# Performance work log

Measured on AMD Instinct MI355X. Metric: run time of the kernel, lower is better.

The kernel has to match this reference:

```python
import jax, jax.numpy as jnp
import numpy as np

K = 512  # number of clusters
D = 128  # feature dim
N = 8192 # number of points


def setup_inputs() -> dict:
    key = jax.random.key(0)
    k1, k2 = jax.random.split(key)
    locF = jax.random.normal(k1, (N, 1, D), dtype=jnp.float32)
    Ck = jax.random.normal(k2, (1, K, D), dtype=jnp.float32)
    return {"locF": locF, "Ck": Ck}


def reference(locF, Ck):
    # locF: [N, 1, D], Ck: [1, K, D]
    x = locF[:, 0, :]          # [N, D]
    c = Ck[0]                  # [K, D]
    # (GEMM expansion avoids the [N, K, D] broadcast; argmin is unchanged)
    d2 = ((x * x).sum(-1, keepdims=True)
          - 2.0 * (x @ c.T)
          + (c * c).sum(-1)[None, :]) / D   # [N, K]
    index = jnp.argmin(d2, axis=1)           # [N]
    # per-cluster scatter-sum and counts (fused, single pass)
    Ck1 = jax.ops.segment_sum(x, index, num_segments=K)[None]  # [1, K, D]
    nItems = jax.ops.segment_sum(jnp.ones((x.shape[0],), dtype=jnp.int32),
                                 index, num_segments=K).reshape(1, -1)  # [1, K]
    return (Ck1, nItems)
```

## Files before the change

### kernel.cpp

```cpp
#include <hip/hip_runtime.h>
#include <hip/hip_bf16.h>

#define KC 512
#define DD 128
#define NP 8192


__global__ __launch_bounds__(256) void kprep(const float* __restrict__ Ck,
                                             float* __restrict__ CkT,
                                             float* __restrict__ sumc2,
                                             float* __restrict__ out) {
    const int b = blockIdx.x;
    const int t = threadIdx.x;
    if (b < 64) {
        const float4 v = *(const float4*)(Ck + b * 1024 + t * 4);
        const int k = b * 8 + (t >> 5);
        const int d = (t & 31) * 4;
        CkT[(d + 0) * KC + k] = v.x;
        CkT[(d + 1) * KC + k] = v.y;
        CkT[(d + 2) * KC + k] = v.z;
        CkT[(d + 3) * KC + k] = v.w;
    } else if (b == 64) {
        #pragma unroll
        for (int c = 0; c < 2; ++c) {
            const int k = t + c * 256;
            const float4* row = (const float4*)(Ck + k * DD);
            float s = 0.f;
            #pragma unroll
            for (int i = 0; i < 32; ++i) {
                const float4 v = row[i];
                s += v.x * v.x + v.y * v.y + v.z * v.z + v.w * v.w;
            }
            sumc2[k] = s;
        }
    } else {
        const int base = (b - 65) * 2048 + t;
        #pragma unroll
        for (int i = 0; i < 8; ++i) {
            const int idx = base + i * 256;
            if (idx < KC * DD + KC) out[idx] = 0.f;
        }
    }
}

__global__ __launch_bounds__(128) void kmain(const float* __restrict__ X,
                                             const float* __restrict__ CkT,
                                             const float* __restrict__ sumc2,
                                             float* __restrict__ out) {
    __shared__ __align__(16) float xs[8 * DD];
    __shared__ float bvx[2][8];
    __shared__ int   bix[2][8];
    __shared__ int   win[8];

    const int tid  = threadIdx.x;
    const int lane = tid & 63;
    const int h    = tid >> 6;
    const int p0   = blockIdx.x * 8;

    {
        const float4* Xv = (const float4*)(X + p0 * DD);
        float4* xv = (float4*)xs;
        xv[tid]       = Xv[tid];
        xv[tid + 128] = Xv[tid + 128];
    }
    __syncthreads();

    const float* cp = CkT + h * 256 + 4 * lane;

    float4 cn[4], cc[4];
    #pragma unroll
    for (int dd = 0; dd < 4; ++dd) cn[dd] = *(const float4*)(cp + dd * KC);

    float acc[8][4];
    #pragma unroll
    for (int p = 0; p < 8; ++p)
        #pragma unroll
        for (int j = 0; j < 4; ++j) acc[p][j] = 0.f;

    #pragma unroll 4
    for (int t = 0; t < 32; ++t) {
        #pragma unroll
        for (int dd = 0; dd < 4; ++dd) cc[dd] = cn[dd];
        if (t < 31) {
            #pragma unroll
            for (int dd = 0; dd < 4; ++dd)
                cn[dd] = *(const float4*)(cp + ((t + 1) * 4 + dd) * KC);
        }
        float4 xf[8];
        #pragma unroll
        for (int p = 0; p < 8; ++p)
            xf[p] = *(const float4*)&xs[p * DD + t * 4];
        #pragma unroll
        for (int dd = 0; dd < 4; ++dd) {
            #pragma unroll
            for (int p = 0; p < 8; ++p) {
                const float xv = (&xf[p].x)[dd];
                acc[p][0] = fmaf(xv, cc[dd].x, acc[p][0]);
                acc[p][1] = fmaf(xv, cc[dd].y, acc[p][1]);
                acc[p][2] = fmaf(xv, cc[dd].z, acc[p][2]);
                acc[p][3] = fmaf(xv, cc[dd].w, acc[p][3]);
            }
        }
    }

    float bestv[8];
    int   besti[8];
    #pragma unroll
    for (int p = 0; p < 8; ++p) { bestv[p] = 3.4e38f; besti[p] = 0; }
    const float4 s2v = *(const float4*)(sumc2 + h * 256 + 4 * lane);
    #pragma unroll
    for (int j = 0; j < 4; ++j) {
        const int cent = h * 256 + 4 * lane + j;
        const float s2 = (&s2v.x)[j];
        #pragma unroll
        for (int p = 0; p < 8; ++p) {
            const float v = fmaf(-2.f, acc[p][j], s2);
            if (v < bestv[p]) { bestv[p] = v; besti[p] = cent; }
        }
    }
    #pragma unroll
    for (int off = 1; off < 64; off <<= 1) {
        #pragma unroll
        for (int p = 0; p < 8; ++p) {
            const float ov = __shfl_xor(bestv[p], off);
            const int   oi = __shfl_xor(besti[p], off);
            if (ov < bestv[p] || (ov == bestv[p] && oi < besti[p])) {
                bestv[p] = ov; besti[p] = oi;
            }
        }
    }
    if (lane == 0) {
        #pragma unroll
        for (int p = 0; p < 8; ++p) { bvx[h][p] = bestv[p]; bix[h][p] = besti[p]; }
    }
    __syncthreads();
    if (tid < 8) {
        const float v0 = bvx[0][tid], v1 = bvx[1][tid];
        win[tid] = (v1 < v0) ? bix[1][tid] : bix[0][tid];
    }
    __syncthreads();

    #pragma unroll
    for (int i = 0; i < 8; ++i) {
        const int flat = tid + 128 * i;
        const int p = flat >> 7;
        const int d = flat & 127;
        atomicAdd(&out[win[p] * DD + d], xs[flat]);
    }
    if (tid < 8) atomicAdd(&out[KC * DD + win[tid]], 1.0f);
}

extern "C" void kernel_launch(void* const* d_in, const int* in_sizes, int n_in,
                              void* d_out, int out_size, void* d_ws, size_t ws_size,
                              hipStream_t stream) {
    const float* locF = (const float*)d_in[0];
    const float* Ck   = (const float*)d_in[1];
    float* out   = (float*)d_out;
    float* sumc2 = (float*)d_ws;
    float* CkT   = (float*)((char*)d_ws + 4096);

    hipLaunchKernelGGL(kprep, dim3(98), dim3(256), 0, stream, Ck, CkT, sumc2, out);
    hipLaunchKernelGGL(kmain, dim3(1024), dim3(128), 0, stream, locF, CkT, sumc2, out);
}
```

Baseline: 41.59 us.

## Retile distance GEMM to 16 points per block with 2 centroids per lane

Each block now handles 16 points with 256 threads, and each lane covers 2 centroids instead of 4, so each centroid value loaded from global memory is reused across twice as many points. The centroid prefetch becomes a two-stage buffer that loads two d-steps ahead. The goal is to halve the CkT global traffic per point and hide load latency better. In exchange the block count is halved, there is a four-way cross-wave reduction, and each thread does more LDS reads per FMA.

```diff
diff --git a/kernel.cpp b/kernel.cpp
--- a/kernel.cpp
+++ b/kernel.cpp
@@ -43,85 +43,89 @@
     }
 }
 
-__global__ __launch_bounds__(128) void kmain(const float* __restrict__ X,
+__global__ __launch_bounds__(256) void kmain(const float* __restrict__ X,
                                              const float* __restrict__ CkT,
                                              const float* __restrict__ sumc2,
                                              float* __restrict__ out) {
-    __shared__ __align__(16) float xs[8 * DD];
-    __shared__ float bvx[2][8];
-    __shared__ int   bix[2][8];
-    __shared__ int   win[8];
+    __shared__ __align__(16) float xs[16 * DD];
+    __shared__ float bvw[4][16];
+    __shared__ int   biw[4][16];
+    __shared__ int   win[16];
 
     const int tid  = threadIdx.x;
     const int lane = tid & 63;
-    const int h    = tid >> 6;
-    const int p0   = blockIdx.x * 8;
+    const int w    = tid >> 6;
+    const int p0   = blockIdx.x * 16;
+    const int c0   = w * 128 + 2 * lane;
 
     {
         const float4* Xv = (const float4*)(X + p0 * DD);
         float4* xv = (float4*)xs;
         xv[tid]       = Xv[tid];
-        xv[tid + 128] = Xv[tid + 128];
+        xv[tid + 256] = Xv[tid + 256];
     }
     __syncthreads();
 
-    const float* cp = CkT + h * 256 + 4 * lane;
+    const float* cp = CkT + c0;
 
-    float4 cn[4], cc[4];
+    float2 cb[2][4];
     #pragma unroll
-    for (int dd = 0; dd < 4; ++dd) cn[dd] = *(const float4*)(cp + dd * KC);
+    for (int dd = 0; dd < 4; ++dd) cb[0][dd] = *(const float2*)(cp + (0 + dd) * KC);
+    #pragma unroll
+    for (int dd = 0; dd < 4; ++dd) cb[1][dd] = *(const float2*)(cp + (4 + dd) * KC);
 
-    float acc[8][4];
+    float acc[16][2];
     #pragma unroll
-    for (int p = 0; p < 8; ++p)
+    for (int p = 0; p < 16; ++p) { acc[p][0] = 0.f; acc[p][1] = 0.f; }
+
+    #pragma unroll 2
+    for (int t = 0; t < 32; ++t) {
+        const int b = t & 1;
+        float2 cc[4];
         #pragma unroll
-        for (int j = 0; j < 4; ++j) acc[p][j] = 0.f;
-
-    #pragma unroll 4
-    for (int t = 0; t < 32; ++t) {
-        #pragma unroll
-        for (int dd = 0; dd < 4; ++dd) cc[dd] = cn[dd];
-        if (t < 31) {
+        for (int dd = 0; dd < 4; ++dd) cc[dd] = cb[b][dd];
+        if (t < 30) {
             #pragma unroll
             for (int dd = 0; dd < 4; ++dd)
-                cn[dd] = *(const float4*)(cp + ((t + 1) * 4 + dd) * KC);
+                cb[b][dd] = *(const float2*)(cp + ((t + 2) * 4 + dd) * KC);
         }
-        float4 xf[8];
         #pragma unroll
-        for (int p = 0; p < 8; ++p)
-            xf[p] = *(const float4*)&xs[p * DD + t * 4];
-        #pragma unroll
-        for (int dd = 0; dd < 4; ++dd) {
+        for (int half = 0; half < 2; ++half) {
+            float4 xf[8];
             #pragma unroll
-            for (int p = 0; p < 8; ++p) {
-                const float xv = (&xf[p].x)[dd];
-                acc[p][0] = fmaf(xv, cc[dd].x, acc[p][0]);
-                acc[p][1] = fmaf(xv, cc[dd].y, acc[p][1]);
-                acc[p][2] = fmaf(xv, cc[dd].z, acc[p][2]);
-                acc[p][3] = fmaf(xv, cc[dd].w, acc[p][3]);
+            for (int i = 0; i < 8; ++i)
+                xf[i] = *(const float4*)&xs[(half * 8 + i) * DD + t * 4];
+            #pragma unroll
+            for (int dd = 0; dd < 4; ++dd) {
+                #pragma unroll
+                for (int i = 0; i < 8; ++i) {
+                    const int p = half * 8 + i;
+                    const float xv = (&xf[i].x)[dd];
+                    acc[p][0] = fmaf(xv, cc[dd].x, acc[p][0]);
+                    acc[p][1] = fmaf(xv, cc[dd].y, acc[p][1]);
+                }
             }
         }
     }
 
-    float bestv[8];
-    int   besti[8];
+    float bestv[16];
+    int   besti[16];
     #pragma unroll
-    for (int p = 0; p < 8; ++p) { bestv[p] = 3.4e38f; besti[p] = 0; }
-    const float4 s2v = *(const float4*)(sumc2 + h * 256 + 4 * lane);
+    for (int p = 0; p < 16; ++p) { bestv[p] = 3.4e38f; besti[p] = 0; }
+    const float2 s2 = *(const float2*)(sumc2 + c0);
     #pragma unroll
-    for (int j = 0; j < 4; ++j) {
-        const int cent = h * 256 + 4 * lane + j;
-        const float s2 = (&s2v.x)[j];
+    for (int j = 0; j < 2; ++j) {
+        const float s2j = (&s2.x)[j];
         #pragma unroll
-        for (int p = 0; p < 8; ++p) {
-            const float v = fmaf(-2.f, acc[p][j], s2);
-            if (v < bestv[p]) { bestv[p] = v; besti[p] = cent; }
+        for (int p = 0; p < 16; ++p) {
+            const float v = fmaf(-2.f, acc[p][j], s2j);
+            if (v < bestv[p]) { bestv[p] = v; besti[p] = c0 + j; }
         }
     }
     #pragma unroll
     for (int off = 1; off < 64; off <<= 1) {
         #pragma unroll
-        for (int p = 0; p < 8; ++p) {
+        for (int p = 0; p < 16; ++p) {
             const float ov = __shfl_xor(bestv[p], off);
             const int   oi = __shfl_xor(besti[p], off);
             if (ov < bestv[p] || (ov == bestv[p] && oi < besti[p])) {
@@ -131,23 +135,30 @@
     }
     if (lane == 0) {
         #pragma unroll
-        for (int p = 0; p < 8; ++p) { bvx[h][p] = bestv[p]; bix[h][p] = besti[p]; }
+        for (int p = 0; p < 16; ++p) { bvw[w][p] = bestv[p]; biw[w][p] = besti[p]; }
     }
     __syncthreads();
-    if (tid < 8) {
-        const float v0 = bvx[0][tid], v1 = bvx[1][tid];
-        win[tid] = (v1 < v0) ? bix[1][tid] : bix[0][tid];
+    if (tid < 16) {
+        float bv = bvw[0][tid];
+        int   bi = biw[0][tid];
+        #pragma unroll
+        for (int w2 = 1; w2 < 4; ++w2) {
+            const float v = bvw[w2][tid];
+            const int   i2 = biw[w2][tid];
+            if (v < bv) { bv = v; bi = i2; }
+        }
+        win[tid] = bi;
     }
     __syncthreads();
 
     #pragma unroll
     for (int i = 0; i < 8; ++i) {
-        const int flat = tid + 128 * i;
+        const int flat = tid + 256 * i;
         const int p = flat >> 7;
         const int d = flat & 127;
         atomicAdd(&out[win[p] * DD + d], xs[flat]);
     }
-    if (tid < 8) atomicAdd(&out[KC * DD + win[tid]], 1.0f);
+    if (tid < 16) atomicAdd(&out[KC * DD + win[tid]], 1.0f);
 }
 
 extern "C" void kernel_launch(void* const* d_in, const int* in_sizes, int n_in,
@@ -160,5 +171,5 @@
     float* CkT   = (float*)((char*)d_ws + 4096);
 
     hipLaunchKernelGGL(kprep, dim3(98), dim3(256), 0, stream, Ck, CkT, sumc2, out);
-    hipLaunchKernelGGL(kmain, dim3(1024), dim3(128), 0, stream, locF, CkT, sumc2, out);
+    hipLaunchKernelGGL(kmain, dim3(512), dim3(256), 0, stream, locF, CkT, sumc2, out);
 }
```

Measured after the change: 50.09 us. 20.4% more time.

## Replace atomic scatter-add with counting-sort and per-cluster gather reduction

Applied to the files above, without the earlier changes.

Removes the per-point global float atomicAdd scatter of feature vectors into cluster sums. The assignment kernel now only writes indices. A single-block kernel builds a histogram and exclusive scan, then buckets point ids by cluster. A gather kernel then sums each cluster's points without atomics. This avoids atomic contention and drops the output zeroing, but adds two launches and a serial single-block ordering stage.

```diff
diff --git a/kernel.cpp b/kernel.cpp
--- a/kernel.cpp
+++ b/kernel.cpp
@@ -8,8 +8,7 @@
 
 __global__ __launch_bounds__(256) void kprep(const float* __restrict__ Ck,
                                              float* __restrict__ CkT,
-                                             float* __restrict__ sumc2,
-                                             float* __restrict__ out) {
+                                             float* __restrict__ sumc2) {
     const int b = blockIdx.x;
     const int t = threadIdx.x;
     if (b < 64) {
@@ -20,7 +19,7 @@
         CkT[(d + 1) * KC + k] = v.y;
         CkT[(d + 2) * KC + k] = v.z;
         CkT[(d + 3) * KC + k] = v.w;
-    } else if (b == 64) {
+    } else {
         #pragma unroll
         for (int c = 0; c < 2; ++c) {
             const int k = t + c * 256;
@@ -33,24 +32,16 @@
             }
             sumc2[k] = s;
         }
-    } else {
-        const int base = (b - 65) * 2048 + t;
-        #pragma unroll
-        for (int i = 0; i < 8; ++i) {
-            const int idx = base + i * 256;
-            if (idx < KC * DD + KC) out[idx] = 0.f;
-        }
-    }
-}
-
-__global__ __launch_bounds__(128) void kmain(const float* __restrict__ X,
-                                             const float* __restrict__ CkT,
-                                             const float* __restrict__ sumc2,
-                                             float* __restrict__ out) {
+    }
+}
+
+__global__ __launch_bounds__(128) void kassign(const float* __restrict__ X,
+                                               const float* __restrict__ CkT,
+                                               const float* __restrict__ sumc2,
+                                               int* __restrict__ idxout) {
     __shared__ __align__(16) float xs[8 * DD];
     __shared__ float bvx[2][8];
     __shared__ int   bix[2][8];
-    __shared__ int   win[8];
 
     const int tid  = threadIdx.x;
     const int lane = tid & 63;
@@ -136,18 +127,80 @@
     __syncthreads();
     if (tid < 8) {
         const float v0 = bvx[0][tid], v1 = bvx[1][tid];
-        win[tid] = (v1 < v0) ? bix[1][tid] : bix[0][tid];
-    }
-    __syncthreads();
-
-    #pragma unroll
-    for (int i = 0; i < 8; ++i) {
-        const int flat = tid + 128 * i;
-        const int p = flat >> 7;
-        const int d = flat & 127;
-        atomicAdd(&out[win[p] * DD + d], xs[flat]);
-    }
-    if (tid < 8) atomicAdd(&out[KC * DD + win[tid]], 1.0f);
+        idxout[p0 + tid] = (v1 < v0) ? bix[1][tid] : bix[0][tid];
+    }
+}
+
+__global__ __launch_bounds__(512) void korder(const int* __restrict__ idx,
+                                              int* __restrict__ order,
+                                              int* __restrict__ cnts,
+                                              int* __restrict__ offs,
+                                              float* __restrict__ out) {
+    __shared__ int hist[KC];
+    __shared__ int scan[KC];
+    __shared__ int cur[KC];
+    const int t = threadIdx.x;
+
+    hist[t] = 0;
+    __syncthreads();
+
+    int myidx[16];
+    #pragma unroll
+    for (int i = 0; i < 16; ++i) {
+        myidx[i] = idx[t + 512 * i];
+        atomicAdd(&hist[myidx[i]], 1);
+    }
+    __syncthreads();
+
+    const int c = hist[t];
+    out[KC * DD + t] = (float)c;
+    cnts[t] = c;
+
+    scan[t] = c;
+    __syncthreads();
+    for (int off = 1; off < KC; off <<= 1) {
+        const int add = (t >= off) ? scan[t - off] : 0;
+        __syncthreads();
+        scan[t] += add;
+        __syncthreads();
+    }
+    const int excl = scan[t] - c;
+    offs[t] = excl;
+    cur[t]  = excl;
+    __syncthreads();
+
+    #pragma unroll
+    for (int i = 0; i < 16; ++i) {
+        const int p = t + 512 * i;
+        const int slot = atomicAdd(&cur[myidx[i]], 1);
+        order[slot] = p;
+    }
+}
+
+__global__ __launch_bounds__(128) void kgather(const float* __restrict__ X,
+                                               const int* __restrict__ order,
+                                               const int* __restrict__ cnts,
+                                               const int* __restrict__ offs,
+                                               float* __restrict__ out) {
+    const int k = blockIdx.x;
+    const int d = threadIdx.x;
+    const int cnt = cnts[k];
+    const int off = offs[k];
+
+    float s0 = 0.f, s1 = 0.f, s2 = 0.f, s3 = 0.f;
+    int i = 0;
+    for (; i + 4 <= cnt; i += 4) {
+        const int pa = order[off + i + 0];
+        const int pb = order[off + i + 1];
+        const int pc = order[off + i + 2];
+        const int pd = order[off + i + 3];
+        s0 += X[pa * DD + d];
+        s1 += X[pb * DD + d];
+        s2 += X[pc * DD + d];
+        s3 += X[pd * DD + d];
+    }
+    for (; i < cnt; ++i) s0 += X[order[off + i] * DD + d];
+    out[k * DD + d] = (s0 + s1) + (s2 + s3);
 }
 
 extern "C" void kernel_launch(void* const* d_in, const int* in_sizes, int n_in,
@@ -156,9 +209,16 @@
     const float* locF = (const float*)d_in[0];
     const float* Ck   = (const float*)d_in[1];
     float* out   = (float*)d_out;
-    float* sumc2 = (float*)d_ws;
-    float* CkT   = (float*)((char*)d_ws + 4096);
-
-    hipLaunchKernelGGL(kprep, dim3(98), dim3(256), 0, stream, Ck, CkT, sumc2, out);
-    hipLaunchKernelGGL(kmain, dim3(1024), dim3(128), 0, stream, locF, CkT, sumc2, out);
-}
+    char*  ws    = (char*)d_ws;
+    float* sumc2 = (float*)(ws);
+    float* CkT   = (float*)(ws + 4096);
+    int*   idx   = (int*)(ws + 266240);
+    int*   order = (int*)(ws + 299008);
+    int*   cnts  = (int*)(ws + 331776);
+    int*   offs  = (int*)(ws + 333824);
+
+    hipLaunchKernelGGL(kprep,   dim3(65),   dim3(256), 0, stream, Ck, CkT, sumc2);
+    hipLaunchKernelGGL(kassign, dim3(1024), dim3(128), 0, stream, locF, CkT, sumc2, idx);
+    hipLaunchKernelGGL(korder,  dim3(1),    dim3(512), 0, stream, idx, order, cnts, offs, out);
+    hipLaunchKernelGGL(kgather, dim3(512),  dim3(128), 0, stream, locF, order, cnts, offs, out);
+}
```

Result: slower. 67.13 us (+61.4%).

## Replace per-point atomic scatter with counting-sort by cluster and segmented gather-sum

Applied to the files above, without the earlier changes.

The old version had every point atomically add its 128 features into its cluster row. This replaces that with a counting sort. The assign kernel records each point's cluster and a rank in per-(cluster, block-group) counters. A single-block scan then builds offsets, the counts output and a sorted (point, cluster) list. A gather kernel sums runs of equal clusters and issues one atomic per run per feature. The aim is to cut float-atomic contention and volume, at the cost of two extra kernel launches and a serial single-block scan.

```diff
diff --git a/kernel.cpp b/kernel.cpp
--- a/kernel.cpp
+++ b/kernel.cpp
@@ -9,7 +9,8 @@
 __global__ __launch_bounds__(256) void kprep(const float* __restrict__ Ck,
                                              float* __restrict__ CkT,
                                              float* __restrict__ sumc2,
-                                             float* __restrict__ out) {
+                                             float* __restrict__ out,
+                                             int* __restrict__ cnts2) {
     const int b = blockIdx.x;
     const int t = threadIdx.x;
     if (b < 64) {
@@ -33,24 +34,26 @@
             }
             sumc2[k] = s;
         }
+    } else if (b < 97) {
+        float* dst = out + (b - 65) * 2048;
+        #pragma unroll
+        for (int i = 0; i < 8; ++i) dst[t + 256 * i] = 0.f;
     } else {
-        const int base = (b - 65) * 2048 + t;
-        #pragma unroll
-        for (int i = 0; i < 8; ++i) {
-            const int idx = base + i * 256;
-            if (idx < KC * DD + KC) out[idx] = 0.f;
-        }
-    }
-}
-
-__global__ __launch_bounds__(128) void kmain(const float* __restrict__ X,
-                                             const float* __restrict__ CkT,
-                                             const float* __restrict__ sumc2,
-                                             float* __restrict__ out) {
+        int* dst = cnts2 + (b - 97) * 2048;
+        #pragma unroll
+        for (int i = 0; i < 8; ++i) dst[t + 256 * i] = 0;
+    }
+}
+
+__global__ __launch_bounds__(128) void kassign(const float* __restrict__ X,
+                                               const float* __restrict__ CkT,
+                                               const float* __restrict__ sumc2,
+                                               int* __restrict__ idxout,
+                                               int* __restrict__ rank2,
+                                               int* __restrict__ cnts2) {
     __shared__ __align__(16) float xs[8 * DD];
     __shared__ float bvx[2][8];
     __shared__ int   bix[2][8];
-    __shared__ int   win[8];
 
     const int tid  = threadIdx.x;
     const int lane = tid & 63;
@@ -136,18 +139,100 @@
     __syncthreads();
     if (tid < 8) {
         const float v0 = bvx[0][tid], v1 = bvx[1][tid];
-        win[tid] = (v1 < v0) ? bix[1][tid] : bix[0][tid];
-    }
-    __syncthreads();
-
+        const int c = (v1 < v0) ? bix[1][tid] : bix[0][tid];
+        const int p = p0 + tid;
+        idxout[p] = c;
+        rank2[p] = atomicAdd(&cnts2[c * 64 + (blockIdx.x & 63)], 1);
+    }
+}
+
+__global__ __launch_bounds__(1024) void kscan(const int* __restrict__ cnts2,
+                                              const int* __restrict__ idx,
+                                              const int* __restrict__ rank2,
+                                              int* __restrict__ offsflat,
+                                              int2* __restrict__ sorted,
+                                              float* __restrict__ out) {
+    __shared__ int sex[1024];
+    const int t = threadIdx.x;
+
+    int arr[32];
+    {
+        const int4* src = (const int4*)cnts2 + t * 8;
+        #pragma unroll
+        for (int i = 0; i < 8; ++i) {
+            const int4 v = src[i];
+            arr[4 * i + 0] = v.x; arr[4 * i + 1] = v.y;
+            arr[4 * i + 2] = v.z; arr[4 * i + 3] = v.w;
+        }
+    }
+    int loc[32];
+    int tot = 0;
+    #pragma unroll
+    for (int i = 0; i < 32; ++i) { loc[i] = tot; tot += arr[i]; }
+
+    sex[t] = tot;
+    __syncthreads();
+    for (int off = 1; off < 1024; off <<= 1) {
+        const int a = (t >= off) ? sex[t - off] : 0;
+        __syncthreads();
+        sex[t] += a;
+        __syncthreads();
+    }
+    const int excl = sex[t] - tot;
+
+    {
+        int4* dst = (int4*)offsflat + t * 8;
+        #pragma unroll
+        for (int i = 0; i < 8; ++i)
+            dst[i] = make_int4(excl + loc[4 * i + 0], excl + loc[4 * i + 1],
+                               excl + loc[4 * i + 2], excl + loc[4 * i + 3]);
+    }
+
+    __syncthreads();
+    sex[t] = excl;
+    __syncthreads();
+    if (t < 512) {
+        const int start = sex[2 * t];
+        const int end   = (t == 511) ? NP : sex[2 * t + 2];
+        out[KC * DD + t] = (float)(end - start);
+    }
+
+    __syncthreads();
     #pragma unroll
     for (int i = 0; i < 8; ++i) {
-        const int flat = tid + 128 * i;
-        const int p = flat >> 7;
-        const int d = flat & 127;
-        atomicAdd(&out[win[p] * DD + d], xs[flat]);
-    }
-    if (tid < 8) atomicAdd(&out[KC * DD + win[tid]], 1.0f);
+        const int p = t + 1024 * i;
+        const int c = idx[p];
+        const int g = (p >> 3) & 63;
+        const int s0 = offsflat[c * 64 + g] + rank2[p];
+        sorted[s0] = make_int2(p, c);
+    }
+}
+
+__global__ __launch_bounds__(128) void kgather(const float* __restrict__ X,
+                                               const int2* __restrict__ sorted,
+                                               float* __restrict__ out) {
+    const int d  = threadIdx.x;
+    const int s0 = blockIdx.x * 16;
+
+    int2 pc[16];
+    #pragma unroll
+    for (int i = 0; i < 16; ++i) pc[i] = sorted[s0 + i];
+
+    float xr[16];
+    #pragma unroll
+    for (int i = 0; i < 16; ++i) xr[i] = X[pc[i].x * DD + d];
+
+    float sum = 0.f;
+    #pragma unroll
+    for (int i = 0; i < 15; ++i) {
+        sum += xr[i];
+        if (pc[i + 1].y != pc[i].y) {
+            atomicAdd(&out[pc[i].y * DD + d], sum);
+            sum = 0.f;
+        }
+    }
+    sum += xr[15];
+    atomicAdd(&out[pc[15].y * DD + d], sum);
 }
 
 extern "C" void kernel_launch(void* const* d_in, const int* in_sizes, int n_in,
@@ -155,10 +240,18 @@
                               hipStream_t stream) {
     const float* locF = (const float*)d_in[0];
     const float* Ck   = (const float*)d_in[1];
-    float* out   = (float*)d_out;
-    float* sumc2 = (float*)d_ws;
-    float* CkT   = (float*)((char*)d_ws + 4096);
-
-    hipLaunchKernelGGL(kprep, dim3(98), dim3(256), 0, stream, Ck, CkT, sumc2, out);
-    hipLaunchKernelGGL(kmain, dim3(1024), dim3(128), 0, stream, locF, CkT, sumc2, out);
-}
+    float* out      = (float*)d_out;
+    char*  ws       = (char*)d_ws;
+    float* sumc2    = (float*)(ws);
+    float* CkT      = (float*)(ws + 4096);
+    int*   idx      = (int*)(ws + 266240);
+    int*   rank2    = (int*)(ws + 299008);
+    int*   cnts2    = (int*)(ws + 331776);
+    int*   offsflat = (int*)(ws + 462848);
+    int2*  sorted   = (int2*)(ws + 593920);
+
+    hipLaunchKernelGGL(kprep,   dim3(113),  dim3(256),  0, stream, Ck, CkT, sumc2, out, cnts2);
+    hipLaunchKernelGGL(kassign, dim3(1024), dim3(128),  0, stream, locF, CkT, sumc2, idx, rank2, cnts2);
+    hipLaunchKernelGGL(kscan,   dim3(1),    dim3(1024), 0, stream, cnts2, idx, rank2, offsflat, sorted, out);
+    hipLaunchKernelGGL(kgather, dim3(512),  dim3(128),  0, stream, locF, sorted, out);
+}
```

Result: slower. 56.64 us (+36.2%).
